# Optimization experiments

Hardware: AMD Instinct MI355X
Metric: run time of the kernel (lower is better)

The kernel has to match this reference:

```python
import jax, jax.numpy as jnp
import numpy as np

VOCAB = 32000
EMBED = 512
HIDDEN = 1024
BATCH = 16
SEQ = 256


def setup_inputs() -> dict:
    key = jax.random.key(0)
    ks = jax.random.split(key, 12)
    E, H, V = EMBED, HIDDEN, VOCAB
    s_gate = 1.0 / np.sqrt(E + H)
    s_out = 1.0 / np.sqrt(H)
    return {
        "input": jax.random.randint(ks[0], (BATCH, SEQ), 0, V, dtype=jnp.int32),
        "embed": jax.random.normal(ks[1], (V, E), dtype=jnp.float32),
        "W_f": jax.random.normal(ks[2], (E + H, H), dtype=jnp.float32) * s_gate,
        "b_f": jax.random.normal(ks[3], (H,), dtype=jnp.float32) * s_gate,
        "W_i": jax.random.normal(ks[4], (E + H, H), dtype=jnp.float32) * s_gate,
        "b_i": jax.random.normal(ks[5], (H,), dtype=jnp.float32) * s_gate,
        "W_c": jax.random.normal(ks[6], (E + H, H), dtype=jnp.float32) * s_gate,
        "b_c": jax.random.normal(ks[7], (H,), dtype=jnp.float32) * s_gate,
        "W_o": jax.random.normal(ks[8], (E + H, H), dtype=jnp.float32) * s_gate,
        "b_o": jax.random.normal(ks[9], (H,), dtype=jnp.float32) * s_gate,
        "W_out": jax.random.normal(ks[10], (H, V), dtype=jnp.float32) * s_out,
        "b_out": jax.random.normal(ks[11], (V,), dtype=jnp.float32) * s_out,
    }


def reference(input, embed, W_f, b_f, W_i, b_i, W_c, b_c, W_o, b_o, W_out, b_out):
    B = input.shape[0]
    H = W_f.shape[1]
    tokens = embed[input]                     # [B, S, E]
    xs = jnp.swapaxes(tokens, 0, 1)           # [S, B, E] for scan over time

    def step(carry, x_t):
        h, c = carry
        catted = jnp.concatenate([x_t, h], axis=1)   # [B, E+H]
        f = jax.nn.sigmoid(catted @ W_f + b_f)
        i = jax.nn.sigmoid(catted @ W_i + b_i)
        cand = jnp.tanh(catted @ W_c + b_c)
        o = jax.nn.sigmoid(catted @ W_o + b_o)
        c = c * f + cand * i
        h = c * o
        return (h, c), h

    h0 = jnp.zeros((B, H), dtype=tokens.dtype)
    c0 = jnp.zeros((B, H), dtype=tokens.dtype)
    _, hs = jax.lax.scan(step, (h0, c0), xs)  # hs: [S, B, H]
    hiddens = jnp.swapaxes(hs, 0, 1)          # [B, S, H]
    return hiddens @ W_out + b_out            # [B, S, V]
```

## Files before the change

### kernel.cpp

```cpp
#include <hip/hip_runtime.h>
#include <hip/hip_bf16.h>

#define VOCAB  32000
#define EMBED  512
#define HIDDEN 1024
#define BATCH  16
#define SEQ    256
#define NROW   (BATCH*SEQ)
#define GCOLS  (4*HIDDEN)
#define NWREC  64
#define NWPACK 192
#define NTILE  8000
#define SENT32 0xFFFFFFFFu

typedef unsigned short u16;
typedef unsigned int   u32;
typedef unsigned long long u64;
typedef __attribute__((ext_vector_type(4))) float f32x4;
typedef __attribute__((ext_vector_type(8))) short bf16x8;
typedef __attribute__((ext_vector_type(8))) unsigned short u16x8;
typedef __attribute__((ext_vector_type(2))) unsigned long long u64x2;

__device__ inline u16 f2bf(float f){
  __hip_bfloat16 h = __float2bfloat16(f);
  return __builtin_bit_cast(u16, h);
}
__device__ inline void gload_lds16(const void* g, void* l){
  __builtin_amdgcn_global_load_lds((const __attribute__((address_space(1))) u32*)g,
                                   (__attribute__((address_space(3))) u32*)l, 16, 0, 0);
}
__device__ __forceinline__ u32 al32(const u32* p){
  return __hip_atomic_load(p, __ATOMIC_RELAXED, __HIP_MEMORY_SCOPE_AGENT);
}
__device__ __forceinline__ u64 al64(const u64* p){
  return __hip_atomic_load(p, __ATOMIC_RELAXED, __HIP_MEMORY_SCOPE_AGENT);
}
__device__ __forceinline__ void as32(u32* p, u32 v){
  __hip_atomic_store(p, v, __ATOMIC_RELAXED, __HIP_MEMORY_SCOPE_AGENT);
}
__device__ __forceinline__ void as64(u64* p, u64 v){
  __hip_atomic_store(p, v, __ATOMIC_RELAXED, __HIP_MEMORY_SCOPE_AGENT);
}

__global__ __launch_bounds__(256) void pack_gates(
    const float* __restrict__ Wf, const float* __restrict__ Wi,
    const float* __restrict__ Wc, const float* __restrict__ Wo,
    const float* __restrict__ bf_, const float* __restrict__ bi_,
    const float* __restrict__ bc_, const float* __restrict__ bo_,
    u16* __restrict__ Wxp, u16* __restrict__ Whp, float* __restrict__ bcat)
{
  const int NT_WX = (GCOLS/16)*(EMBED/32)*64;
  const int NT_WH = (GCOLS/16)*(HIDDEN/32)*64;
  int t = blockIdx.x*256 + threadIdx.x;
  if (t < NT_WX){
    int u = t;
    int lane = u&63; int kb = (u>>6)&15; int nblk = u>>10;
    int col = nblk*16 + (lane&15);
    int k0  = kb*32 + ((lane>>4)<<3);
    int g = col>>10, j = col&1023;
    const float* W = (g==0)?Wf:(g==1)?Wi:(g==2)?Wc:Wo;
    u16x8 v;
    #pragma unroll
    for (int e=0;e<8;e++) v[e] = f2bf(W[(size_t)(k0+e)*HIDDEN + j]);
    *(u16x8*)(Wxp + (size_t)u*8) = v;
  } else if (t < NT_WX + NT_WH){
    int u = t - NT_WX;
    int lane = u&63; int kb = (u>>6)&31; int nblk = u>>11;
    int col = nblk*16 + (lane&15);
    int k0  = kb*32 + ((lane>>4)<<3);
    int g = col>>10, j = col&1023;
    const float* W = (g==0)?Wf:(g==1)?Wi:(g==2)?Wc:Wo;
    u16x8 v;
    #pragma unroll
    for (int e=0;e<8;e++) v[e] = f2bf(W[(size_t)(EMBED + k0+e)*HIDDEN + j]);
    *(u16x8*)(Whp + (size_t)u*8) = v;
  } else {
    int u = t - NT_WX - NT_WH;
    if (u < GCOLS){
      int g = u>>10, j = u&1023;
      const float* B = (g==0)?bf_:(g==1)?bi_:(g==2)?bc_:bo_;
      bcat[u] = B[j];
    }
  }
}

__global__ __launch_bounds__(256) void gather_kernel(
    const int* __restrict__ tok, const float* __restrict__ embed, u16* __restrict__ Xg)
{
  int t = blockIdx.x*256 + threadIdx.x;
  int lane = t&63; int kb = (t>>6)&15; int mblk = t>>10;
  int s = mblk; int b = lane&15;
  int token = tok[b*SEQ + s];
  int k0 = kb*32 + ((lane>>4)<<3);
  const float* src = embed + (size_t)token*EMBED + k0;
  u16x8 v;
  #pragma unroll
  for (int e=0;e<8;e++) v[e] = f2bf(src[e]);
  *(u16x8*)(Xg + (size_t)t*8) = v;
}

template<int KB, bool REMAP>
__global__ __launch_bounds__(256,2) void gemm_pk(
    const u16* __restrict__ Ap, const u16* __restrict__ Bp,
    const float* __restrict__ bias, float* __restrict__ C,
    int Nblk128, int N)
{
  __shared__ u16 sm[8192];
  int tid = threadIdx.x; int lane = tid&63; int wv = tid>>6;
  int nwg = gridDim.x;
  int bid = blockIdx.x;
  int swz = (bid&7)*(nwg>>3) + (bid>>3);
  int bm = swz / Nblk128, bn = swz % Nblk128;
  int wr = wv>>1, wc = wv&1;
  f32x4 acc[4][4] = {};
  const u16* Abase = Ap + (size_t)(bm*8)*KB*512;
  const u16* Bbase = Bp + (size_t)(bn*8)*KB*512;
  for (int kb=0; kb<KB; ++kb){
    __syncthreads();
    #pragma unroll
    for (int c2=0;c2<4;c2++){
      int chunk = wv*4 + c2;
      const u16* g;
      if (chunk < 8) g = Abase + ((size_t)chunk*KB + kb)*512 + lane*8;
      else           g = Bbase + ((size_t)(chunk-8)*KB + kb)*512 + lane*8;
      gload_lds16(g, sm + chunk*512);
    }
    __syncthreads();
    bf16x8 a[4], b[4];
    #pragma unroll
    for (int m=0;m<4;m++) a[m] = *(const bf16x8*)(sm + (wr*4+m)*512 + lane*8);
    #pragma unroll
    for (int n=0;n<4;n++) b[n] = *(const bf16x8*)(sm + 4096 + (wc*4+n)*512 + lane*8);
    #pragma unroll
    for (int m=0;m<4;m++)
      #pragma unroll
      for (int n=0;n<4;n++)
        acc[m][n] = __builtin_amdgcn_mfma_f32_16x16x32_bf16(a[m], b[n], acc[m][n], 0,0,0);
  }
  int colb = bn*128 + wc*64;
  int rowb = bm*128 + wr*64;
  #pragma unroll
  for (int m=0;m<4;m++){
    int row0 = rowb + m*16 + (lane>>4)*4;
    #pragma unroll
    for (int n=0;n<4;n++){
      int col = colb + n*16 + (lane&15);
      float bv = bias[col];
      #pragma unroll
      for (int r2=0;r2<4;r2++){
        int row = row0 + r2;
        int orow = REMAP ? ((row&15)*SEQ + (row>>4)) : row;
        C[(size_t)orow*N + col] = acc[m][n][r2] + bv;
      }
    }
  }
}

__global__ __launch_bounds__(256,1) void lstm_fused(
    const u16* __restrict__ Whp, const float* __restrict__ Xpre,
    u16* hb, u16* Hp, u32* cnt, u32* tix, u32* packdone,
    const float* __restrict__ Wout, u16* __restrict__ Woutp,
    const float* __restrict__ bout, float* __restrict__ out)
{
  __shared__ char SMEM[148480];
  __shared__ u32 s_tick;
  u16* smWf = (u16*)SMEM;
  float (*gl)[16][17] = (float (*)[16][17])(SMEM + 131072);
  u16* sm = (u16*)SMEM;

  int tid = threadIdx.x; int lane = tid&63; int v = tid>>6;
  int w = blockIdx.x;

  if (w >= NWREC){
    const int NPK = (VOCAB/16)*(HIDDEN/32)*64;
    int u0 = (w - NWREC)*256 + tid;
    for (int u = u0; u < NPK; u += NWPACK*256){
      int l = u&63; int kb = (u>>6)&31; int nblk = u>>11;
      int col = nblk*16 + (l&15);
      int k0  = kb*32 + ((l>>4)<<3);
      u16x8 vv;
      #pragma unroll
      for (int e=0;e<8;e++) vv[e] = f2bf(Wout[(size_t)(k0+e)*VOCAB + col]);
      u64x2 t2 = __builtin_bit_cast(u64x2, vv);
      u64* dst = (u64*)(Woutp + (size_t)u*8);
      as64(dst+0, t2[0]);
      as64(dst+1, t2[1]);
    }
    asm volatile("s_waitcnt vmcnt(0)" ::: "memory");
    __syncthreads();
    if (tid==0) (void)__hip_atomic_fetch_add(packdone, 1u,
                       __ATOMIC_RELAXED, __HIP_MEMORY_SCOPE_AGENT);
  } else {
    #pragma unroll
    for (int f=0; f<32; ++f){
      int frag = v*32 + f;
      int g = frag>>5, kc = frag&31;
      const u16* src = Whp + ((size_t)(g*64 + w)*32 + kc)*512 + lane*8;
      gload_lds16(src, smWf + (size_t)frag*512);
    }
    asm volatile("s_waitcnt vmcnt(0)" ::: "memory");
    __syncthreads();

    float c = 0.f;
    int pb = tid>>4, pj = tid&15;
    int j = w*16 + pj;
    const int a_row = lane&15, a_k = (lane>>4)*8;
    const float* xb0 = Xpre + (size_t)pb*GCOLS + j;
    float x0 = xb0[0], x1 = xb0[1024], x2 = xb0[2048], x3 = xb0[3072];

    for (int s=0;s<SEQ;s++){
      const u16* rbuf = hb + (size_t)s*16384;
      u64 vv[16];
      #pragma unroll
      for (int i=0;i<16;i++){
        const u64* p = (const u64*)(rbuf + a_row*1024 + (v*8+(i>>1))*32 + a_k) + (i&1);
        vv[i] = al64(p);
      }
      for(;;){
        bool ok = true;
        #pragma unroll
        for (int i=0;i<16;i++)
          if (((u32)vv[i]==SENT32) | ((u32)(vv[i]>>32)==SENT32)) ok = false;
        if (ok) break;
        __builtin_amdgcn_s_sleep(1);
        #pragma unroll
        for (int i=0;i<16;i++){
          if (((u32)vv[i]==SENT32) | ((u32)(vv[i]>>32)==SENT32)){
            const u64* p = (const u64*)(rbuf + a_row*1024 + (v*8+(i>>1))*32 + a_k) + (i&1);
            vv[i] = al64(p);
          }
        }
      }
      bf16x8 af[8];
      #pragma unroll
      for (int i=0;i<8;i++){
        u64x2 t2 = {vv[2*i], vv[2*i+1]};
        af[i] = __builtin_bit_cast(bf16x8, t2);
      }
      f32x4 acc[4] = {};
      #pragma unroll
      for (int i=0;i<8;i++){
        #pragma unroll
        for (int g=0;g<4;g++){
          bf16x8 wfv = *(const bf16x8*)(smWf + ((size_t)(g*32 + v*8 + i))*512 + lane*8);
          acc[g] = __builtin_amdgcn_mfma_f32_16x16x32_bf16(af[i], wfv, acc[g], 0,0,0);
        }
      }
      {
        int jj = lane&15, b0 = (lane>>4)*4;
        #pragma unroll
        for (int g=0;g<4;g++)
          #pragma unroll
          for (int r2=0;r2<4;r2++)
            gl[v*4+g][b0+r2][jj] = acc[g][r2];
      }
      __syncthreads();
      float p0 = x0 + gl[0][pb][pj] + gl[4][pb][pj] + gl[ 8][pb][pj] + gl[12][pb][pj];
      float p1 = x1 + gl[1][pb][pj] + gl[5][pb][pj] + gl[ 9][pb][pj] + gl[13][pb][pj];
      float p2 = x2 + gl[2][pb][pj] + gl[6][pb][pj] + gl[10][pb][pj] + gl[14][pb][pj];
      float p3 = x3 + gl[3][pb][pj] + gl[7][pb][pj] + gl[11][pb][pj] + gl[15][pb][pj];
      float fg = 1.f/(1.f+__expf(-p0));
      float ig = 1.f/(1.f+__expf(-p1));
      float e2 = __expf(2.f*fminf(fmaxf(p2,-15.f),15.f));
      float cand = (e2-1.f)/(e2+1.f);
      float og = 1.f/(1.f+__expf(-p3));
      c = c*fg + cand*ig;
      float h = c*og;
      if (s < SEQ-1){
        const float* xn = Xpre + ((size_t)(s+1)*16 + pb)*GCOLS + j;
        x0 = xn[0]; x1 = xn[1024]; x2 = xn[2048]; x3 = xn[3072];
      }
      u32 hw_ = (u32)f2bf(h);
      u32 ow_ = (u32)__shfl_xor((int)hw_, 1);
      if ((pj&1)==0){
        u32 word = hw_ | (ow_<<16);
        if (s < SEQ-1){
          u16* wstep = hb + (size_t)(s+1)*16384;
          as32((u32*)wstep + (size_t)pb*512 + w*8 + (pj>>1), word);
        }
        as32((u32*)Hp + (size_t)s*8192 + (size_t)(j>>5)*256
                      + (size_t)(((j>>3)&3)*16 + pb)*4 + ((j&7)>>1), word);
      }
      asm volatile("s_waitcnt vmcnt(0)" ::: "memory");
      __syncthreads();
      if (tid==0)
        (void)__hip_atomic_fetch_add(cnt + (size_t)s*16, 1u,
                 __ATOMIC_RELAXED, __HIP_MEMORY_SCOPE_AGENT);
    }
  }

  if (tid==0){
    while (al32(packdone) < (u32)NWPACK) __builtin_amdgcn_s_sleep(2);
  }
  __syncthreads();

  int wv = tid>>6;
  int wr = wv>>1, wc = wv&1;
  for(;;){
    __syncthreads();
    if (tid==0) s_tick = __hip_atomic_fetch_add(tix, 1u,
                   __ATOMIC_RELAXED, __HIP_MEMORY_SCOPE_AGENT);
    __syncthreads();
    u32 t = s_tick;
    if (t >= (u32)NTILE) break;
    int bm = (int)(t/250u), bn = (int)(t%250u);
    if (tid==0){
      while (al32(cnt + (size_t)(bm*8+7)*16) < (u32)NWREC)
        __builtin_amdgcn_s_sleep(2);
    }
    __syncthreads();
    f32x4 acc[4][4] = {};
    const u16* Abase = Hp + (size_t)(bm*8)*32*512;
    const u16* Bbase = Woutp + (size_t)(bn*8)*32*512;
    for (int kb=0; kb<32; ++kb){
      __syncthreads();
      #pragma unroll
      for (int c2=0;c2<4;c2++){
        int chunk = wv*4 + c2;
        const u16* g;
        if (chunk < 8) g = Abase + ((size_t)chunk*32 + kb)*512 + lane*8;
        else           g = Bbase + ((size_t)(chunk-8)*32 + kb)*512 + lane*8;
        gload_lds16(g, sm + chunk*512);
      }
      __syncthreads();
      bf16x8 a[4], b[4];
      #pragma unroll
      for (int m=0;m<4;m++) a[m] = *(const bf16x8*)(sm + (wr*4+m)*512 + lane*8);
      #pragma unroll
      for (int n=0;n<4;n++) b[n] = *(const bf16x8*)(sm + 4096 + (wc*4+n)*512 + lane*8);
      #pragma unroll
      for (int m=0;m<4;m++)
        #pragma unroll
        for (int n=0;n<4;n++)
          acc[m][n] = __builtin_amdgcn_mfma_f32_16x16x32_bf16(a[m], b[n], acc[m][n], 0,0,0);
    }
    int colb = bn*128 + wc*64;
    int rowb = bm*128 + wr*64;
    #pragma unroll
    for (int m=0;m<4;m++){
      int row0 = rowb + m*16 + (lane>>4)*4;
      #pragma unroll
      for (int n=0;n<4;n++){
        int col = colb + n*16 + (lane&15);
        float bv = bout[col];
        #pragma unroll
        for (int r2=0;r2<4;r2++){
          int row = row0 + r2;
          int orow = (row&15)*SEQ + (row>>4);
          out[(size_t)orow*VOCAB + col] = acc[m][n][r2] + bv;
        }
      }
    }
  }
}

extern "C" void kernel_launch(void* const* d_in, const int* in_sizes, int n_in,
                              void* d_out, int out_size, void* d_ws, size_t ws_size,
                              hipStream_t stream)
{
  (void)in_sizes; (void)n_in; (void)out_size; (void)ws_size;
  const int*   tok   = (const int*)d_in[0];
  const float* embed = (const float*)d_in[1];
  const float* Wf    = (const float*)d_in[2];
  const float* bf_   = (const float*)d_in[3];
  const float* Wi    = (const float*)d_in[4];
  const float* bi_   = (const float*)d_in[5];
  const float* Wc    = (const float*)d_in[6];
  const float* bc_   = (const float*)d_in[7];
  const float* Wo    = (const float*)d_in[8];
  const float* bo_   = (const float*)d_in[9];
  const float* Wout  = (const float*)d_in[10];
  const float* bout  = (const float*)d_in[11];
  float* out = (float*)d_out;

  char* ws = (char*)d_ws;
  size_t off = 0;
  auto alloc = [&](size_t bytes)->void*{
    void* p = ws + off; off += (bytes + 255) & ~(size_t)255; return p;
  };
  u16*  Wxp   = (u16*)alloc((size_t)2097152*2);
  u16*  Xg    = (u16*)alloc((size_t)2097152*2);
  float* bcat = (float*)alloc((size_t)4096*4);
  u16*  hb    = (u16*)ws;
  u16*  Whp   = (u16*)alloc((size_t)4194304*2);
  u16*  Woutp = (u16*)alloc((size_t)32768000*2);
  float* Xpre = (float*)alloc((size_t)NROW*GCOLS*4);
  u16*  Hp    = (u16*)alloc((size_t)4194304*2);
  u32*  cnt   = (u32*)alloc((size_t)256*64);
  u32*  tix   = (u32*)alloc((size_t)256);
  u32*  packdone = (u32*)alloc((size_t)256);

  pack_gates<<<3088, 256, 0, stream>>>(Wf,Wi,Wc,Wo, bf_,bi_,bc_,bo_,
                                       Wxp, Whp, bcat);
  gather_kernel<<<1024, 256, 0, stream>>>(tok, embed, Xg);
  gemm_pk<16,false><<<1024, 256, 0, stream>>>(Xg, Wxp, bcat, Xpre, 32, GCOLS);
  (void)hipMemsetAsync(hb, 0x00, 32768, stream);
  (void)hipMemsetAsync((char*)hb + 32768, 0xFF, 255*32768, stream);
  (void)hipMemsetAsync(cnt, 0, 256*64 + 512, stream);
  lstm_fused<<<NWREC+NWPACK, 256, 0, stream>>>(Whp, Xpre, hb, Hp, cnt, tix,
                                               packdone, Wout, Woutp, bout, out);
}
```

Before: 1.250 ms.

## Relax per-step recurrence sync, batch counters, triple-buffer output GEMM

```diff
diff --git a/kernel.cpp b/kernel.cpp
--- a/kernel.cpp
+++ b/kernel.cpp
@@ -158,7 +158,7 @@
 
 __global__ __launch_bounds__(256,1) void lstm_fused(
     const u16* __restrict__ Whp, const float* __restrict__ Xpre,
-    u16* hb, u16* Hp, u32* cnt, u32* tix, u32* packdone,
+    u16* hb, u16* Hp, u32* cnt, u32* tix, u32* packdone, u32* fl,
     const float* __restrict__ Wout, u16* __restrict__ Woutp,
     const float* __restrict__ bout, float* __restrict__ out)
 {
@@ -166,7 +166,7 @@
   __shared__ u32 s_tick;
   u16* smWf = (u16*)SMEM;
   float (*gl)[16][17] = (float (*)[16][17])(SMEM + 131072);
-  u16* sm = (u16*)SMEM;
+  u16* smg = (u16*)SMEM;
 
   int tid = threadIdx.x; int lane = tid&63; int v = tid>>6;
   int w = blockIdx.x;
@@ -216,19 +216,31 @@
         const u64* p = (const u64*)(rbuf + a_row*1024 + (v*8+(i>>1))*32 + a_k) + (i&1);
         vv[i] = al64(p);
       }
-      for(;;){
-        bool ok = true;
-        #pragma unroll
-        for (int i=0;i<16;i++)
-          if (((u32)vv[i]==SENT32) | ((u32)(vv[i]>>32)==SENT32)) ok = false;
-        if (ok) break;
-        __builtin_amdgcn_s_sleep(1);
-        #pragma unroll
-        for (int i=0;i<16;i++){
-          if (((u32)vv[i]==SENT32) | ((u32)(vv[i]>>32)==SENT32)){
+      bool ok = true;
+      #pragma unroll
+      for (int i=0;i<16;i++)
+        ok &= ((u32)vv[i]!=SENT32) & ((u32)(vv[i]>>32)!=SENT32);
+      if (!ok){
+        if (s > 0){
+          const u32* fls = fl + (size_t)s*64;
+          for(;;){
+            u32 fv = al32(fls + lane);
+            if (__all(fv != 0u)) break;
+            __builtin_amdgcn_s_sleep(1);
+          }
+        }
+        for(;;){
+          #pragma unroll
+          for (int i=0;i<16;i++){
             const u64* p = (const u64*)(rbuf + a_row*1024 + (v*8+(i>>1))*32 + a_k) + (i&1);
             vv[i] = al64(p);
           }
+          bool ok2 = true;
+          #pragma unroll
+          for (int i=0;i<16;i++)
+            ok2 &= ((u32)vv[i]!=SENT32) & ((u32)(vv[i]>>32)!=SENT32);
+          if (ok2) break;
+          __builtin_amdgcn_s_sleep(1);
         }
       }
       bf16x8 af[8];
@@ -281,11 +293,16 @@
         as32((u32*)Hp + (size_t)s*8192 + (size_t)(j>>5)*256
                       + (size_t)(((j>>3)&3)*16 + pb)*4 + ((j&7)>>1), word);
       }
-      asm volatile("s_waitcnt vmcnt(0)" ::: "memory");
       __syncthreads();
-      if (tid==0)
-        (void)__hip_atomic_fetch_add(cnt + (size_t)s*16, 1u,
-                 __ATOMIC_RELAXED, __HIP_MEMORY_SCOPE_AGENT);
+      if (tid==0 && s < SEQ-1)
+        as32(fl + (size_t)(s+1)*64 + w, 1u);
+      if ((s&7)==7){
+        asm volatile("s_waitcnt vmcnt(0)" ::: "memory");
+        __syncthreads();
+        if (tid==0)
+          (void)__hip_atomic_fetch_add(cnt + (size_t)(s>>3)*16, 1u,
+                   __ATOMIC_RELAXED, __HIP_MEMORY_SCOPE_AGENT);
+      }
     }
   }
 
@@ -305,29 +322,35 @@
     if (t >= (u32)NTILE) break;
     int bm = (int)(t/250u), bn = (int)(t%250u);
     if (tid==0){
-      while (al32(cnt + (size_t)(bm*8+7)*16) < (u32)NWREC)
+      while (al32(cnt + (size_t)bm*16) < (u32)NWREC)
         __builtin_amdgcn_s_sleep(2);
     }
     __syncthreads();
-    f32x4 acc[4][4] = {};
-    const u16* Abase = Hp + (size_t)(bm*8)*32*512;
-    const u16* Bbase = Woutp + (size_t)(bn*8)*32*512;
-    for (int kb=0; kb<32; ++kb){
-      __syncthreads();
+    const u16* Ab = Hp + (size_t)(bm*8)*32*512;
+    const u16* Bb = Woutp + (size_t)(bn*8)*32*512;
+    auto stage = [&](int kb, int bi){
       #pragma unroll
       for (int c2=0;c2<4;c2++){
         int chunk = wv*4 + c2;
         const u16* g;
-        if (chunk < 8) g = Abase + ((size_t)chunk*32 + kb)*512 + lane*8;
-        else           g = Bbase + ((size_t)(chunk-8)*32 + kb)*512 + lane*8;
-        gload_lds16(g, sm + chunk*512);
-      }
-      __syncthreads();
+        if (chunk < 8) g = Ab + ((size_t)chunk*32 + kb)*512 + lane*8;
+        else           g = Bb + ((size_t)(chunk-8)*32 + kb)*512 + lane*8;
+        gload_lds16(g, smg + (size_t)bi*8192 + chunk*512);
+      }
+    };
+    stage(0,0); stage(1,1);
+    f32x4 acc[4][4] = {};
+    for (int kb=0; kb<32; ++kb){
+      if (kb<31) asm volatile("s_waitcnt vmcnt(4)" ::: "memory");
+      else       asm volatile("s_waitcnt vmcnt(0)" ::: "memory");
+      __builtin_amdgcn_s_barrier();
+      if (kb+2<32) stage(kb+2, (kb+2)%3);
+      const u16* bufp = smg + (size_t)(kb%3)*8192;
       bf16x8 a[4], b[4];
       #pragma unroll
-      for (int m=0;m<4;m++) a[m] = *(const bf16x8*)(sm + (wr*4+m)*512 + lane*8);
-      #pragma unroll
-      for (int n=0;n<4;n++) b[n] = *(const bf16x8*)(sm + 4096 + (wc*4+n)*512 + lane*8);
+      for (int m=0;m<4;m++) a[m] = *(const bf16x8*)(bufp + (wr*4+m)*512 + lane*8);
+      #pragma unroll
+      for (int n=0;n<4;n++) b[n] = *(const bf16x8*)(bufp + 4096 + (wc*4+n)*512 + lane*8);
       #pragma unroll
       for (int m=0;m<4;m++)
         #pragma unroll
@@ -347,7 +370,8 @@
         for (int r2=0;r2<4;r2++){
           int row = row0 + r2;
           int orow = (row&15)*SEQ + (row>>4);
-          out[(size_t)orow*VOCAB + col] = acc[m][n][r2] + bv;
+          __builtin_nontemporal_store(acc[m][n][r2] + bv,
+                                      &out[(size_t)orow*VOCAB + col]);
         }
       }
     }
@@ -386,9 +410,10 @@
   u16*  Woutp = (u16*)alloc((size_t)32768000*2);
   float* Xpre = (float*)alloc((size_t)NROW*GCOLS*4);
   u16*  Hp    = (u16*)alloc((size_t)4194304*2);
-  u32*  cnt   = (u32*)alloc((size_t)256*64);
+  u32*  cnt   = (u32*)alloc((size_t)4096);
   u32*  tix   = (u32*)alloc((size_t)256);
   u32*  packdone = (u32*)alloc((size_t)256);
+  u32*  fl    = (u32*)alloc((size_t)SEQ*64*4);
 
   pack_gates<<<3088, 256, 0, stream>>>(Wf,Wi,Wc,Wo, bf_,bi_,bc_,bo_,
                                        Wxp, Whp, bcat);
@@ -396,7 +421,7 @@
   gemm_pk<16,false><<<1024, 256, 0, stream>>>(Xg, Wxp, bcat, Xpre, 32, GCOLS);
   (void)hipMemsetAsync(hb, 0x00, 32768, stream);
   (void)hipMemsetAsync((char*)hb + 32768, 0xFF, 255*32768, stream);
-  (void)hipMemsetAsync(cnt, 0, 256*64 + 512, stream);
+  (void)hipMemsetAsync(cnt, 0, 4096 + 256 + 256 + SEQ*64*4, stream);
   lstm_fused<<<NWREC+NWPACK, 256, 0, stream>>>(Whp, Xpre, hb, Hp, cnt, tix,
-                                               packdone, Wout, Woutp, bout, out);
-}
+                                               packdone, fl, Wout, Woutp, bout, out);
+}
```

New measurement: 1.248 ms. About the same (-0.1%).
